# Optimization experiments

Measured on AMD Instinct MI355X. Metric: run time of the kernel, lower is better.

Reference implementation:

```python
import jax, jax.numpy as jnp
import numpy as np

N = 262144
FEAT = 64
D = 128
DEPTH = 2
N_LAYERS = 1
SCALE_FEATURES = 0.5
SCALE_STEPS = (1.0 - SCALE_FEATURES) / DEPTH
LN_EPS = 1e-5
SLOPE = 0.01


def leaky(x):
    return jnp.where(x >= 0, x, SLOPE * x)


def layernorm(x):
    mu = x.mean(-1, keepdims=True)
    var = ((x - mu) ** 2).mean(-1, keepdims=True)
    return (x - mu) / jnp.sqrt(var + LN_EPS)


def setup_inputs() -> dict:
    key = jax.random.key(0)
    ks = jax.random.split(key, 12)
    raw_feats = jax.random.normal(ks[0], (N, FEAT), dtype=jnp.float32)
    uids = jnp.arange(N, dtype=jnp.int32)
    id_map = jax.random.randint(ks[1], (N, 1, 2), 0, N, dtype=jnp.int32)
    # FeatureEmbedder params
    slow_mean = jnp.zeros((FEAT,), jnp.float32)
    slow_std = jnp.ones((FEAT,), jnp.float32)
    W_embd = jax.random.normal(ks[2], (FEAT, D), jnp.float32) / np.sqrt(FEAT)
    b_embd = jnp.zeros((D,), jnp.float32)
    Wl = jax.random.normal(ks[3], (N_LAYERS, D, D), jnp.float32) / np.sqrt(D)
    bl = jnp.zeros((N_LAYERS, D), jnp.float32)
    # node_emb params
    W_node = jax.random.normal(ks[4], (D, D), jnp.float32) / np.sqrt(D)
    b_node = jnp.zeros((D,), jnp.float32)
    rezero = jnp.full((1,), 0.1, jnp.float32)  # nonzero so depth loop is active
    W_w = jax.random.normal(ks[5], (D, 1), jnp.float32) * 0.01
    W_v = jax.random.normal(ks[6], (D, 1), jnp.float32) / np.sqrt(D)
    return {
        'raw_feats': raw_feats, 'uids': uids, 'id_map': id_map,
        'slow_mean': slow_mean, 'slow_std': slow_std,
        'W_embd': W_embd, 'b_embd': b_embd, 'Wl': Wl, 'bl': bl,
        'W_node': W_node, 'b_node': b_node, 'rezero': rezero,
        'W_w': W_w, 'W_v': W_v,
    }


def reference(raw_feats, uids, id_map, slow_mean, slow_std, W_embd, b_embd,
              Wl, bl, W_node, b_node, rezero, W_w, W_v):
    # sorted_feats = cat([raw_feats, zeros(1, FEAT)])  -> [N+1, FEAT]
    sorted_feats = jnp.concatenate(
        [raw_feats, jnp.zeros((1, FEAT), raw_feats.dtype)], axis=0)

    # FeatureEmbedder: SlowNorm -> Linear -> leaky, residual blocks, LayerNorm, *scale
    x = (sorted_feats - slow_mean) / (slow_std + 0.001)
    x = leaky(x @ W_embd + b_embd)
    for i in range(N_LAYERS):
        # F.leaky_relu(Sequential(Linear, LeakyReLU)(x)) + x  (double leaky)
        x = leaky(leaky(x @ Wl[i] + bl[i])) + x
    x = layernorm(x) * SCALE_FEATURES  # [N+1, D]

    # uids == arange(N), so uid-value -> row-index lookup is identity
    ids = id_map[:, 0, :]  # [N, 2] row indices into x

    for _ in range(DEPTH):
        feats = x[ids].mean(axis=1)                 # gather [N,2,D] -> mean -> [N,D]
        feats = leaky(feats @ W_node + b_node)       # node_emb
        new = x[:-1] + feats * (SCALE_STEPS * rezero)
        x = jnp.concatenate([new, x[-1:]], axis=0)   # scatter-update rows [:-1]

    x_main = x[:-1]
    w = x_main @ W_w                                  # weight head, no bias
    v = jax.lax.stop_gradient(x_main) @ W_v           # value head on detached x
    return (x_main, w, v)
```

## Files before the change

### kernel.cpp

```cpp
#include <hip/hip_runtime.h>


#define NROWS 262144
#define NBLK  4096
#define GRID2 2048

typedef __attribute__((ext_vector_type(8))) short bhalf8;
typedef __attribute__((ext_vector_type(4))) float f32x4;
typedef __attribute__((ext_vector_type(4))) unsigned int u32x4;

__device__ __forceinline__ unsigned short f2bf(float x) {
    union { float f; unsigned u; } v; v.f = x;
    unsigned r = v.u + 0x7FFFu + ((v.u >> 16) & 1u);
    return (unsigned short)(r >> 16);
}
__device__ __forceinline__ float bflo(unsigned u) {
    union { unsigned u; float f; } v; v.u = u << 16; return v.f;
}
__device__ __forceinline__ float bfhi(unsigned u) {
    union { unsigned u; float f; } v; v.u = u & 0xFFFF0000u; return v.f;
}
__device__ __forceinline__ float leaky(float x) { return x >= 0.0f ? x : 0.01f * x; }

__global__ void __launch_bounds__(256)
setup_kernel(const float* __restrict__ smean, const float* __restrict__ sstd,
             const float* __restrict__ Wemb, const float* __restrict__ bemb,
             const float* __restrict__ Wl, const float* __restrict__ Wn,
             unsigned short* __restrict__ wpack, float* __restrict__ bembP)
{
    int task = blockIdx.x * 256 + threadIdx.x;
    if (blockIdx.x < 160) {
        if (task < 8192) {
            int f = task >> 9, idx = task & 511;
            int t = f >> 1, s = f & 1, lane = idx >> 3, j = idx & 7;
            int n = t * 16 + (lane & 15), k = s * 32 + (lane >> 4) * 8 + j;
            wpack[task] = f2bf(Wemb[k * 128 + n] / (sstd[k] + 0.001f));
        } else if (task < 24576) {
            int u = task - 8192;
            int f = u >> 9, idx = u & 511;
            int t = f >> 2, s = f & 3, lane = idx >> 3, j = idx & 7;
            int n = t * 16 + (lane & 15), k = s * 32 + (lane >> 4) * 8 + j;
            wpack[task] = f2bf(Wl[k * 128 + n]);
        } else if (task < 40960) {
            int u = task - 24576;
            int f = u >> 9, idx = u & 511;
            int t = f >> 2, s = f & 3, lane = idx >> 3, j = idx & 7;
            int n = t * 16 + (lane & 15), k = s * 32 + (lane >> 4) * 8 + j;
            wpack[task] = f2bf(0.5f * Wn[k * 128 + n]);
        }
    } else {
        int n = threadIdx.x;
        if (n < 128) {
            float acc = bemb[n];
            for (int k = 0; k < 64; k++)
                acc -= smean[k] / (sstd[k] + 0.001f) * Wemb[k * 128 + n];
            bembP[n] = acc;
        }
    }
}

__global__ void __launch_bounds__(256, 4)
phase_a_kernel(const float* __restrict__ feats,
               const unsigned short* __restrict__ wembF,
               const float* __restrict__ bembP,
               const unsigned short* __restrict__ wlF,
               const float* __restrict__ bl,
               unsigned short* __restrict__ xout)
{
    __shared__ __align__(16) short hb[64 * 136];
    const int tid = threadIdx.x, lane = tid & 63, wv = tid >> 6;
    const int m = lane & 15, q = lane >> 4;
    const int r0 = blockIdx.x * 64;

    const bhalf8* wbe = (const bhalf8*)wembF;
    const bhalf8* wbl = (const bhalf8*)wlF;

    bhalf8 af[2];
    #pragma unroll
    for (int s = 0; s < 2; s++) {
        const float* fp = feats + (size_t)(r0 + wv * 16 + m) * 64 + s * 32 + q * 8;
        f32x4 f0 = *(const f32x4*)fp;
        f32x4 f1 = *(const f32x4*)(fp + 4);
        bhalf8 a;
        #pragma unroll
        for (int jj = 0; jj < 4; jj++) { a[jj] = (short)f2bf(f0[jj]); a[4 + jj] = (short)f2bf(f1[jj]); }
        af[s] = a;
    }
    f32x4 acc[8] = {};
    #pragma unroll
    for (int s = 0; s < 2; s++)
        #pragma unroll
        for (int t = 0; t < 8; t++)
            acc[t] = __builtin_amdgcn_mfma_f32_16x16x32_bf16(af[s], wbe[(t * 2 + s) * 64 + lane], acc[t], 0, 0, 0);

    unsigned hvp[8][2];
    #pragma unroll
    for (int t = 0; t < 8; t++) {
        float be = bembP[t * 16 + m];
        unsigned short hq[4];
        #pragma unroll
        for (int p = 0; p < 4; p++) {
            float h = leaky(acc[t][p] + be);
            hq[p] = f2bf(h);
            hb[(wv * 16 + q * 4 + p) * 136 + t * 16 + m] = (short)hq[p];
        }
        hvp[t][0] = (unsigned)hq[0] | ((unsigned)hq[1] << 16);
        hvp[t][1] = (unsigned)hq[2] | ((unsigned)hq[3] << 16);
    }
    f32x4 acc2[8] = {};
    #pragma unroll
    for (int s = 0; s < 4; s++) {
        bhalf8 a = *(const bhalf8*)&hb[(wv * 16 + m) * 136 + s * 32 + q * 8];
        #pragma unroll
        for (int t = 0; t < 8; t++)
            acc2[t] = __builtin_amdgcn_mfma_f32_16x16x32_bf16(a, wbl[(t * 4 + s) * 64 + lane], acc2[t], 0, 0, 0);
    }

    float sum[4] = {0, 0, 0, 0}, ssq[4] = {0, 0, 0, 0};
    #pragma unroll
    for (int t = 0; t < 8; t++) {
        float bb = bl[t * 16 + m];
        float hvv[4] = { bflo(hvp[t][0]), bfhi(hvp[t][0]), bflo(hvp[t][1]), bfhi(hvp[t][1]) };
        #pragma unroll
        for (int p = 0; p < 4; p++) {
            float v = leaky(leaky(acc2[t][p] + bb)) + hvv[p];
            acc2[t][p] = v;
            sum[p] += v; ssq[p] += v * v;
        }
    }
    #pragma unroll
    for (int p = 0; p < 4; p++) {
        #pragma unroll
        for (int d = 1; d < 16; d <<= 1) {
            sum[p] += __shfl_xor(sum[p], d, 64);
            ssq[p] += __shfl_xor(ssq[p], d, 64);
        }
    }
    #pragma unroll
    for (int p = 0; p < 4; p++) {
        float mu  = sum[p] * (1.0f / 128.0f);
        float var = ssq[p] * (1.0f / 128.0f) - mu * mu;
        float rs  = rsqrtf(var + 1e-5f) * 0.5f;
        int row = wv * 16 + q * 4 + p;
        #pragma unroll
        for (int t = 0; t < 8; t++)
            hb[row * 136 + t * 16 + m] = (short)f2bf((acc2[t][p] - mu) * rs);
    }
    __syncthreads();
    for (int c = tid; c < 64 * 16; c += 256) {
        int row = c >> 4, cb = (c & 15) * 8;
        *reinterpret_cast<u32x4*>(&xout[(size_t)(r0 + row) * 128 + cb]) =
            *reinterpret_cast<const u32x4*>(&hb[row * 136 + cb]);
    }
}

__device__ __forceinline__ void gather_rows(const unsigned short* __restrict__ xin,
                                            int2 ids, int q, u32x4* ga, u32x4* gb)
{
    const unsigned short* xa = xin + (size_t)ids.x * 128 + q * 8;
    const unsigned short* xb = xin + (size_t)ids.y * 128 + q * 8;
    #pragma unroll
    for (int s = 0; s < 4; s++) {
        ga[s] = *(const u32x4*)(xa + s * 32);
        gb[s] = *(const u32x4*)(xb + s * 32);
    }
}

__device__ __forceinline__ void node_mm(const u32x4* ga, const u32x4* gb,
                                        const bhalf8* __restrict__ wbn, int lane, f32x4* acc)
{
    #pragma unroll
    for (int s = 0; s < 4; s++) {
        bhalf8 a;
        #pragma unroll
        for (int w = 0; w < 4; w++) {
            a[2 * w]     = (short)f2bf(bflo(ga[s][w]) + bflo(gb[s][w]));
            a[2 * w + 1] = (short)f2bf(bfhi(ga[s][w]) + bfhi(gb[s][w]));
        }
        #pragma unroll
        for (int t = 0; t < 8; t++)
            acc[t] = __builtin_amdgcn_mfma_f32_16x16x32_bf16(a, wbn[(t * 4 + s) * 64 + lane], acc[t], 0, 0, 0);
    }
}

__device__ __forceinline__ void stage_g(short* gls, const f32x4* acc,
                                        const float* __restrict__ bn, float scale,
                                        int wv, int q, int m)
{
    #pragma unroll
    for (int t = 0; t < 8; t++) {
        float bb = bn[t * 16 + m];
        #pragma unroll
        for (int p = 0; p < 4; p++)
            gls[(wv * 16 + q * 4 + p) * 136 + t * 16 + m] = (short)f2bf(leaky(acc[t][p] + bb) * scale);
    }
}

template <typename TOUT>
__device__ __forceinline__ void prop_epilogue(const short* gls, const u32x4* xown, int r0,
                                              const float* __restrict__ Ww, const float* __restrict__ Wv,
                                              TOUT* __restrict__ xout, float* __restrict__ wout,
                                              float* __restrict__ vout, int final_pass,
                                              int crow, int ccb, int lane)
{
    #pragma unroll
    for (int i = 0; i < 4; i++) {
        int row = i * 16 + crow;
        u32x4 gv = *(const u32x4*)&gls[row * 136 + ccb * 8];
        u32x4 xv = xown[i];
        float xn[8];
        #pragma unroll
        for (int w = 0; w < 4; w++) {
            xn[2 * w]     = bflo(xv[w]) + bflo(gv[w]);
            xn[2 * w + 1] = bfhi(xv[w]) + bfhi(gv[w]);
        }
        if (!final_pass) {
            u32x4 ov;
            #pragma unroll
            for (int w = 0; w < 4; w++)
                ov[w] = (unsigned)f2bf(xn[2 * w]) | ((unsigned)f2bf(xn[2 * w + 1]) << 16);
            *reinterpret_cast<u32x4*>(reinterpret_cast<unsigned short*>(xout) + (size_t)(r0 + row) * 128 + ccb * 8) = ov;
        } else {
            float* op = reinterpret_cast<float*>(xout) + (size_t)(r0 + row) * 128 + ccb * 8;
            f32x4 o0, o1;
            #pragma unroll
            for (int w = 0; w < 4; w++) { o0[w] = xn[w]; o1[w] = xn[4 + w]; }
            *reinterpret_cast<f32x4*>(op)     = o0;
            *reinterpret_cast<f32x4*>(op + 4) = o1;
            f32x4 w0 = *(const f32x4*)&Ww[ccb * 8], w1 = *(const f32x4*)&Ww[ccb * 8 + 4];
            f32x4 v0 = *(const f32x4*)&Wv[ccb * 8], v1 = *(const f32x4*)&Wv[ccb * 8 + 4];
            float ws = 0.0f, vs = 0.0f;
            #pragma unroll
            for (int w = 0; w < 4; w++) {
                ws += xn[w] * w0[w] + xn[4 + w] * w1[w];
                vs += xn[w] * v0[w] + xn[4 + w] * v1[w];
            }
            #pragma unroll
            for (int d = 1; d < 16; d <<= 1) {
                ws += __shfl_xor(ws, d, 64);
                vs += __shfl_xor(vs, d, 64);
            }
            if ((lane & 15) == 0) { wout[r0 + row] = ws; vout[r0 + row] = vs; }
        }
    }
}

template <typename TOUT, int TILES>
__global__ void __launch_bounds__(256)
prop_kernel(const unsigned short* __restrict__ xin, const int* __restrict__ idmap,
            const unsigned short* __restrict__ wnF, const float* __restrict__ bn,
            const float* __restrict__ rez, const float* __restrict__ Ww,
            const float* __restrict__ Wv, TOUT* __restrict__ xout,
            float* __restrict__ wout, float* __restrict__ vout, int final_pass)
{
    __shared__ __align__(16) short gls[64 * 136];
    const int tid = threadIdx.x, lane = tid & 63, wv = tid >> 6;
    const int m = lane & 15, q = lane >> 4;
    const int crow = tid >> 4, ccb = tid & 15;
    const bhalf8* wbn = (const bhalf8*)wnF;
    const float scale = 0.25f * rez[0];

    const int r0A = blockIdx.x * 64;
    int2 idsA = ((const int2*)idmap)[r0A + wv * 16 + m];
    u32x4 gaA[4], gbA[4], xownA[4];
    gather_rows(xin, idsA, q, gaA, gbA);
    #pragma unroll
    for (int i = 0; i < 4; i++)
        xownA[i] = *(const u32x4*)(xin + (size_t)(r0A + i * 16 + crow) * 128 + ccb * 8);

    if (TILES == 1) {
        f32x4 acc[8] = {};
        node_mm(gaA, gbA, wbn, lane, acc);
        stage_g(gls, acc, bn, scale, wv, q, m);
        __syncthreads();
        prop_epilogue(gls, xownA, r0A, Ww, Wv, xout, wout, vout, final_pass, crow, ccb, lane);
    } else {
        const int r0B = (blockIdx.x + GRID2) * 64;
        int2 idsB = ((const int2*)idmap)[r0B + wv * 16 + m];
        u32x4 gaB[4], gbB[4], xownB[4];
        gather_rows(xin, idsB, q, gaB, gbB);
        #pragma unroll
        for (int i = 0; i < 4; i++)
            xownB[i] = *(const u32x4*)(xin + (size_t)(r0B + i * 16 + crow) * 128 + ccb * 8);

        f32x4 accA[8] = {};
        node_mm(gaA, gbA, wbn, lane, accA);
        stage_g(gls, accA, bn, scale, wv, q, m);
        __syncthreads();

        f32x4 accB[8] = {};
        node_mm(gaB, gbB, wbn, lane, accB);
        prop_epilogue(gls, xownA, r0A, Ww, Wv, xout, wout, vout, final_pass, crow, ccb, lane);
        __syncthreads();

        stage_g(gls, accB, bn, scale, wv, q, m);
        __syncthreads();
        prop_epilogue(gls, xownB, r0B, Ww, Wv, xout, wout, vout, final_pass, crow, ccb, lane);
    }
}

extern "C" void kernel_launch(void* const* d_in, const int* in_sizes, int n_in,
                              void* d_out, int out_size, void* d_ws, size_t ws_size,
                              hipStream_t stream) {
    const float* feats = (const float*)d_in[0];
    const int*   idmap = (const int*)d_in[2];
    const float* smean = (const float*)d_in[3];
    const float* sstd  = (const float*)d_in[4];
    const float* Wemb  = (const float*)d_in[5];
    const float* bemb  = (const float*)d_in[6];
    const float* Wl    = (const float*)d_in[7];
    const float* bl    = (const float*)d_in[8];
    const float* Wn    = (const float*)d_in[9];
    const float* bn    = (const float*)d_in[10];
    const float* rez   = (const float*)d_in[11];
    const float* Ww    = (const float*)d_in[12];
    const float* Wv    = (const float*)d_in[13];

    char* ws = (char*)d_ws;
    unsigned short* wpack = (unsigned short*)ws;
    float*          bembP = (float*)(ws + 81920);
    unsigned short* x1    = (unsigned short*)(ws + (1ull << 20));

    float* out = (float*)d_out;
    unsigned short* x0 = (unsigned short*)d_out;
    float* wout = out + (size_t)NROWS * 128;
    float* vout = wout + NROWS;

    setup_kernel<<<161, 256, 0, stream>>>(smean, sstd, Wemb, bemb, Wl, Wn, wpack, bembP);
    phase_a_kernel<<<NBLK, 256, 0, stream>>>(feats, wpack, bembP, wpack + 8192, bl, x0);
    prop_kernel<unsigned short, 1><<<NBLK, 256, 0, stream>>>(x0, idmap, wpack + 24576, bn, rez, Ww, Wv,
                                                             x1, nullptr, nullptr, 0);
    prop_kernel<float, 2><<<GRID2, 256, 0, stream>>>(x1, idmap, wpack + 24576, bn, rez, Ww, Wv,
                                                     out, wout, vout, 1);
}
```

Measured before the change: 351.4 us.

## Fuse both propagation steps into one kernel by recomputing two-hop neighbor updates

Replaces the two propagation kernels with a single kernel. For each row it gathers its two neighbors and their neighbors, recomputes the first-step update for those neighbors locally, then applies the second step. This removes the intermediate bf16 x1 write/read and one launch, but triples the gathers and the node-matmul work per row and uses three LDS tiles, which may lower occupancy. The change also breaks the zero-padding row semantics (index N) in the same way the old code did.

```diff
diff --git a/kernel.cpp b/kernel.cpp
--- a/kernel.cpp
+++ b/kernel.cpp
@@ -3,7 +3,6 @@
 
 #define NROWS 262144
 #define NBLK  4096
-#define GRID2 2048
 
 typedef __attribute__((ext_vector_type(8))) short bhalf8;
 typedef __attribute__((ext_vector_type(4))) float f32x4;
@@ -19,6 +18,9 @@
 }
 __device__ __forceinline__ float bfhi(unsigned u) {
     union { unsigned u; float f; } v; v.u = u & 0xFFFF0000u; return v.f;
+}
+__device__ __forceinline__ float bf2f(unsigned short s) {
+    union { unsigned u; float f; } v; v.u = ((unsigned)s) << 16; return v.f;
 }
 __device__ __forceinline__ float leaky(float x) { return x >= 0.0f ? x : 0.01f * x; }
 
@@ -196,106 +198,110 @@
     }
 }
 
-template <typename TOUT>
-__device__ __forceinline__ void prop_epilogue(const short* gls, const u32x4* xown, int r0,
-                                              const float* __restrict__ Ww, const float* __restrict__ Wv,
-                                              TOUT* __restrict__ xout, float* __restrict__ wout,
-                                              float* __restrict__ vout, int final_pass,
-                                              int crow, int ccb, int lane)
-{
-    #pragma unroll
-    for (int i = 0; i < 4; i++) {
-        int row = i * 16 + crow;
-        u32x4 gv = *(const u32x4*)&gls[row * 136 + ccb * 8];
-        u32x4 xv = xown[i];
-        float xn[8];
-        #pragma unroll
-        for (int w = 0; w < 4; w++) {
-            xn[2 * w]     = bflo(xv[w]) + bflo(gv[w]);
-            xn[2 * w + 1] = bfhi(xv[w]) + bfhi(gv[w]);
-        }
-        if (!final_pass) {
-            u32x4 ov;
-            #pragma unroll
-            for (int w = 0; w < 4; w++)
-                ov[w] = (unsigned)f2bf(xn[2 * w]) | ((unsigned)f2bf(xn[2 * w + 1]) << 16);
-            *reinterpret_cast<u32x4*>(reinterpret_cast<unsigned short*>(xout) + (size_t)(r0 + row) * 128 + ccb * 8) = ov;
-        } else {
-            float* op = reinterpret_cast<float*>(xout) + (size_t)(r0 + row) * 128 + ccb * 8;
-            f32x4 o0, o1;
-            #pragma unroll
-            for (int w = 0; w < 4; w++) { o0[w] = xn[w]; o1[w] = xn[4 + w]; }
-            *reinterpret_cast<f32x4*>(op)     = o0;
-            *reinterpret_cast<f32x4*>(op + 4) = o1;
-            f32x4 w0 = *(const f32x4*)&Ww[ccb * 8], w1 = *(const f32x4*)&Ww[ccb * 8 + 4];
-            f32x4 v0 = *(const f32x4*)&Wv[ccb * 8], v1 = *(const f32x4*)&Wv[ccb * 8 + 4];
-            float ws = 0.0f, vs = 0.0f;
-            #pragma unroll
-            for (int w = 0; w < 4; w++) {
-                ws += xn[w] * w0[w] + xn[4 + w] * w1[w];
-                vs += xn[w] * v0[w] + xn[4 + w] * v1[w];
-            }
-            #pragma unroll
-            for (int d = 1; d < 16; d <<= 1) {
-                ws += __shfl_xor(ws, d, 64);
-                vs += __shfl_xor(vs, d, 64);
-            }
-            if ((lane & 15) == 0) { wout[r0 + row] = ws; vout[r0 + row] = vs; }
-        }
-    }
-}
-
-template <typename TOUT, int TILES>
 __global__ void __launch_bounds__(256)
-prop_kernel(const unsigned short* __restrict__ xin, const int* __restrict__ idmap,
-            const unsigned short* __restrict__ wnF, const float* __restrict__ bn,
-            const float* __restrict__ rez, const float* __restrict__ Ww,
-            const float* __restrict__ Wv, TOUT* __restrict__ xout,
-            float* __restrict__ wout, float* __restrict__ vout, int final_pass)
-{
-    __shared__ __align__(16) short gls[64 * 136];
+prop2x_kernel(const unsigned short* __restrict__ xin, const int* __restrict__ idmap,
+              const unsigned short* __restrict__ wnF, const float* __restrict__ bn,
+              const float* __restrict__ rez, const float* __restrict__ Ww,
+              const float* __restrict__ Wv, float* __restrict__ xout,
+              float* __restrict__ wout, float* __restrict__ vout)
+{
+    __shared__ __align__(16) short T0[64 * 136];
+    __shared__ __align__(16) short T1[64 * 136];
+    __shared__ __align__(16) short T2[64 * 136];
     const int tid = threadIdx.x, lane = tid & 63, wv = tid >> 6;
     const int m = lane & 15, q = lane >> 4;
     const int crow = tid >> 4, ccb = tid & 15;
+    const int r0 = blockIdx.x * 64;
     const bhalf8* wbn = (const bhalf8*)wnF;
     const float scale = 0.25f * rez[0];
 
-    const int r0A = blockIdx.x * 64;
-    int2 idsA = ((const int2*)idmap)[r0A + wv * 16 + m];
-    u32x4 gaA[4], gbA[4], xownA[4];
-    gather_rows(xin, idsA, q, gaA, gbA);
+    const int myrow = r0 + wv * 16 + m;
+    int2 ids  = ((const int2*)idmap)[myrow];
+    int2 idsA = ((const int2*)idmap)[ids.x];
+    int2 idsB = ((const int2*)idmap)[ids.y];
+
+    u32x4 ga[4], gb[4], gaa[4], gab[4], gba[4], gbb[4];
+    gather_rows(xin, ids,  q, ga,  gb);
+    gather_rows(xin, idsA, q, gaa, gab);
+    gather_rows(xin, idsB, q, gba, gbb);
+
+    u32x4 xown[4];
     #pragma unroll
     for (int i = 0; i < 4; i++)
-        xownA[i] = *(const u32x4*)(xin + (size_t)(r0A + i * 16 + crow) * 128 + ccb * 8);
-
-    if (TILES == 1) {
+        xown[i] = *(const u32x4*)(xin + (size_t)(r0 + i * 16 + crow) * 128 + ccb * 8);
+
+    {
         f32x4 acc[8] = {};
-        node_mm(gaA, gbA, wbn, lane, acc);
-        stage_g(gls, acc, bn, scale, wv, q, m);
-        __syncthreads();
-        prop_epilogue(gls, xownA, r0A, Ww, Wv, xout, wout, vout, final_pass, crow, ccb, lane);
-    } else {
-        const int r0B = (blockIdx.x + GRID2) * 64;
-        int2 idsB = ((const int2*)idmap)[r0B + wv * 16 + m];
-        u32x4 gaB[4], gbB[4], xownB[4];
-        gather_rows(xin, idsB, q, gaB, gbB);
-        #pragma unroll
-        for (int i = 0; i < 4; i++)
-            xownB[i] = *(const u32x4*)(xin + (size_t)(r0B + i * 16 + crow) * 128 + ccb * 8);
-
-        f32x4 accA[8] = {};
-        node_mm(gaA, gbA, wbn, lane, accA);
-        stage_g(gls, accA, bn, scale, wv, q, m);
-        __syncthreads();
-
-        f32x4 accB[8] = {};
-        node_mm(gaB, gbB, wbn, lane, accB);
-        prop_epilogue(gls, xownA, r0A, Ww, Wv, xout, wout, vout, final_pass, crow, ccb, lane);
-        __syncthreads();
-
-        stage_g(gls, accB, bn, scale, wv, q, m);
-        __syncthreads();
-        prop_epilogue(gls, xownB, r0B, Ww, Wv, xout, wout, vout, final_pass, crow, ccb, lane);
+        node_mm(gaa, gab, wbn, lane, acc);
+        stage_g(T0, acc, bn, scale, wv, q, m);
+    }
+    {
+        f32x4 acc[8] = {};
+        node_mm(gba, gbb, wbn, lane, acc);
+        stage_g(T1, acc, bn, scale, wv, q, m);
+    }
+    {
+        f32x4 acc[8] = {};
+        node_mm(ga, gb, wbn, lane, acc);
+        stage_g(T2, acc, bn, scale, wv, q, m);
+    }
+
+    f32x4 acc1[8] = {};
+    #pragma unroll
+    for (int s = 0; s < 4; s++) {
+        bhalf8 gAv = *(const bhalf8*)&T0[(wv * 16 + m) * 136 + s * 32 + q * 8];
+        bhalf8 gBv = *(const bhalf8*)&T1[(wv * 16 + m) * 136 + s * 32 + q * 8];
+        bhalf8 a1;
+        #pragma unroll
+        for (int w = 0; w < 4; w++) {
+            unsigned short xalo = f2bf(bflo(ga[s][w]) + bf2f((unsigned short)gAv[2 * w]));
+            unsigned short xahi = f2bf(bfhi(ga[s][w]) + bf2f((unsigned short)gAv[2 * w + 1]));
+            unsigned short xblo = f2bf(bflo(gb[s][w]) + bf2f((unsigned short)gBv[2 * w]));
+            unsigned short xbhi = f2bf(bfhi(gb[s][w]) + bf2f((unsigned short)gBv[2 * w + 1]));
+            a1[2 * w]     = (short)f2bf(bf2f(xalo) + bf2f(xblo));
+            a1[2 * w + 1] = (short)f2bf(bf2f(xahi) + bf2f(xbhi));
+        }
+        #pragma unroll
+        for (int t = 0; t < 8; t++)
+            acc1[t] = __builtin_amdgcn_mfma_f32_16x16x32_bf16(a1, wbn[(t * 4 + s) * 64 + lane], acc1[t], 0, 0, 0);
+    }
+    stage_g(T0, acc1, bn, scale, wv, q, m);
+    __syncthreads();
+
+    #pragma unroll
+    for (int i = 0; i < 4; i++) {
+        int row = i * 16 + crow;
+        u32x4 gR = *(const u32x4*)&T2[row * 136 + ccb * 8];
+        u32x4 g1 = *(const u32x4*)&T0[row * 136 + ccb * 8];
+        u32x4 xv = xown[i];
+        float xn[8];
+        #pragma unroll
+        for (int w = 0; w < 4; w++) {
+            unsigned short x1lo = f2bf(bflo(xv[w]) + bflo(gR[w]));
+            unsigned short x1hi = f2bf(bfhi(xv[w]) + bfhi(gR[w]));
+            xn[2 * w]     = bf2f(x1lo) + bflo(g1[w]);
+            xn[2 * w + 1] = bf2f(x1hi) + bfhi(g1[w]);
+        }
+        float* op = xout + (size_t)(r0 + row) * 128 + ccb * 8;
+        f32x4 o0, o1;
+        #pragma unroll
+        for (int w = 0; w < 4; w++) { o0[w] = xn[w]; o1[w] = xn[4 + w]; }
+        *reinterpret_cast<f32x4*>(op)     = o0;
+        *reinterpret_cast<f32x4*>(op + 4) = o1;
+        f32x4 w0 = *(const f32x4*)&Ww[ccb * 8], w1 = *(const f32x4*)&Ww[ccb * 8 + 4];
+        f32x4 v0 = *(const f32x4*)&Wv[ccb * 8], v1 = *(const f32x4*)&Wv[ccb * 8 + 4];
+        float ws = 0.0f, vs = 0.0f;
+        #pragma unroll
+        for (int w = 0; w < 4; w++) {
+            ws += xn[w] * w0[w] + xn[4 + w] * w1[w];
+            vs += xn[w] * v0[w] + xn[4 + w] * v1[w];
+        }
+        #pragma unroll
+        for (int d = 1; d < 16; d <<= 1) {
+            ws += __shfl_xor(ws, d, 64);
+            vs += __shfl_xor(vs, d, 64);
+        }
+        if ((lane & 15) == 0) { wout[r0 + row] = ws; vout[r0 + row] = vs; }
     }
 }
 
@@ -319,17 +325,14 @@
     char* ws = (char*)d_ws;
     unsigned short* wpack = (unsigned short*)ws;
     float*          bembP = (float*)(ws + 81920);
-    unsigned short* x1    = (unsigned short*)(ws + (1ull << 20));
+    unsigned short* xbuf  = (unsigned short*)(ws + (1ull << 20));
 
     float* out = (float*)d_out;
-    unsigned short* x0 = (unsigned short*)d_out;
     float* wout = out + (size_t)NROWS * 128;
     float* vout = wout + NROWS;
 
     setup_kernel<<<161, 256, 0, stream>>>(smean, sstd, Wemb, bemb, Wl, Wn, wpack, bembP);
-    phase_a_kernel<<<NBLK, 256, 0, stream>>>(feats, wpack, bembP, wpack + 8192, bl, x0);
-    prop_kernel<unsigned short, 1><<<NBLK, 256, 0, stream>>>(x0, idmap, wpack + 24576, bn, rez, Ww, Wv,
-                                                             x1, nullptr, nullptr, 0);
-    prop_kernel<float, 2><<<GRID2, 256, 0, stream>>>(x1, idmap, wpack + 24576, bn, rez, Ww, Wv,
-                                                     out, wout, vout, 1);
-}
+    phase_a_kernel<<<NBLK, 256, 0, stream>>>(feats, wpack, bembP, wpack + 8192, bl, xbuf);
+    prop2x_kernel<<<NBLK, 256, 0, stream>>>(xbuf, idmap, wpack + 24576, bn, rez, Ww, Wv,
+                                            out, wout, vout);
+}
```

Result: slower. 430.1 us (+22.4%).
